# Kernel tuning notes

Measured on AMD Instinct MI355X. Metric: run time of the kernel, lower is better.

## Reference

```python
import jax, jax.numpy as jnp
import numpy as np

# decoded layout constants
NN, NO, SD = 16, 8, 4          # num_neighbors, num_obstacles, state_dim_per_agent
B = 131072                      # batch rows
H1, E, HP, AD = 64, 16, 64, 2   # phi hidden, embed, psi hidden, action dim
D_ROBOT, D_OBST = 0.3, 0.3
B_GAMMA, B_EXPH = 0.05, 1.0
PHI_MIN, PHI_MAX = -2.0, 2.0
A_MAX = 2.0


def setup_inputs() -> dict:
    key = jax.random.key(0)
    kx, kw = jax.random.split(key)
    # x: [count | goal(SD) | NN neighbor rel-states (SD each) | NO obstacle rel-pos (2 each)]
    x = jax.random.normal(kx, (B, 1 + SD + SD * NN + 2 * NO), dtype=jnp.float32) * 2.0
    x = x.at[:, 0].set(float(NN))
    names = [("Wp1n", (SD, H1)), ("bp1n", (H1,)), ("Wp2n", (H1, E)), ("bp2n", (E,)),
             ("Wr1n", (E, H1)), ("br1n", (H1,)), ("Wr2n", (H1, E)), ("br2n", (E,)),
             ("Wp1o", (2, H1)), ("bp1o", (H1,)), ("Wp2o", (H1, E)), ("bp2o", (E,)),
             ("Wr1o", (E, H1)), ("br1o", (H1,)), ("Wr2o", (H1, E)), ("br2o", (E,)),
             ("Wpsi1", (2 * E + SD, HP)), ("bpsi1", (HP,)), ("Wpsi2", (HP, AD)), ("bpsi2", (AD,))]
    ks = jax.random.split(kw, len(names))
    inp = {"x": x}
    for (n, sh), k in zip(names, ks):
        s = 1.0 / np.sqrt(sh[0])  # torch Linear default init scale
        inp[n] = jax.random.uniform(k, sh, jnp.float32, -s, s)
    return inp


def _mlp2(h, W1, b1, W2, b2):
    # Feedforward: activation between layers, linear output
    return jax.nn.relu(h @ W1 + b1) @ W2 + b2


def _deepset(el, Wp1, bp1, Wp2, bp2, Wr1, br1, Wr2, br2):
    # el: [B, n, d] -> phi each element, sum over set, rho
    phi = _mlp2(el, Wp1, bp1, Wp2, bp2)          # [B, n, E]
    return _mlp2(phi.sum(axis=1), Wr1, br1, Wr2, br2)  # [B, E]


def _barrier_sum(P, D):
    # P: [B, n, 2]; APF barrier gamma * P / (|P| * (|P|-D)^exph), summed over n
    nrm = jnp.linalg.norm(P, axis=-1, keepdims=True)   # [B, n, 1]
    H = nrm - D
    return (B_GAMMA * P / (nrm * H ** B_EXPH)).sum(axis=1)  # [B, 2]


def reference(x, Wp1n, bp1n, Wp2n, bp2n, Wr1n, br1n, Wr2n, br2n,
              Wp1o, bp1o, Wp2o, bp2o, Wr1o, br1o, Wr2o, br2o,
              Wpsi1, bpsi1, Wpsi2, bpsi2):
    nb = x.shape[0]
    g = x[:, 1:1 + SD]                                        # goal
    nbr = x[:, 1 + SD:1 + SD + SD * NN].reshape(nb, NN, SD)   # neighbor rel-states
    obs = x[:, 1 + SD + SD * NN:].reshape(nb, NO, 2)          # obstacle rel-pos

    rho_n = _deepset(nbr, Wp1n, bp1n, Wp2n, bp2n, Wr1n, br1n, Wr2n, br2n)
    rho_o = _deepset(obs, Wp1o, bp1o, Wp2o, bp2o, Wr1o, br1o, Wr2o, br2o)

    h = jnp.concatenate([rho_n, rho_o, g], axis=1)            # [B, 2E+SD]
    emp = _mlp2(h, Wpsi1, bpsi1, Wpsi2, bpsi2)                # psi network
    emp = (jnp.tanh(emp) + 1.0) / 2.0 * (PHI_MAX - PHI_MIN) + PHI_MIN  # scale_empty

    bar = _barrier_sum(-nbr[:, :, :2], D_ROBOT) + _barrier_sum(-obs, D_OBST)

    action = emp + bar
    # scale(): divide rows whose inf-norm exceeds a_max
    inv_alpha = jnp.maximum(jnp.max(jnp.abs(action), axis=1, keepdims=True) / A_MAX, 1.0)
    return action / inv_alpha
```

## Files before the change

### kernel.cpp

```cpp
#include <hip/hip_runtime.h>
#include <math.h>


typedef __attribute__((ext_vector_type(8))) _Float16 f16x8;
typedef __attribute__((ext_vector_type(2))) __fp16 fp16x2;
typedef __attribute__((ext_vector_type(4))) float f32x4;

#define XW 85

#define FR_S1N  0
#define FR_S1O  4
#define FR_G2N  8
#define FR_G2O  10
#define FR_RNA  12
#define FR_RNB  16
#define FR_ROA  18
#define FR_ROB  22
#define FR_PSI1 24
#define FR_PSI2 32
#define N_FRAGS 34

#define BIG_STR 144
#define PHI_STR 80
#define CAT_STR 144
#define L_BIG 0
#define L_PHI 2304
#define L_CAT 3584
#define L_OUT 5888
#define L_BAR 6016
#define WAVE_LDS 6144

__device__ __forceinline__ float fast_rcp(float x)  { return __builtin_amdgcn_rcpf(x); }
__device__ __forceinline__ float fast_sqrt(float x) { return __builtin_amdgcn_sqrtf(x); }

__device__ __forceinline__ float two_tanh(float a) {
    float ax = fabsf(a);
    float e = __expf(2.0f * ax);
    float t = 1.0f - 2.0f * fast_rcp(e + 1.0f);
    return copysignf(2.0f * t, a);
}

__device__ __forceinline__ void lds_fence() {
    __asm__ __volatile__("s_waitcnt lgkmcnt(0)" ::: "memory");
}

__device__ __forceinline__ unsigned pk2(float a, float b) {
    union { fp16x2 h; unsigned u; } t;
    t.h = __builtin_amdgcn_cvt_pkrtz(a, b);
    return t.u;
}
__device__ __forceinline__ f16x8 make_a4(float f0, float f1, float f2, float f3) {
    union { unsigned u[4]; f16x8 v; } U;
    U.u[0] = pk2(f0, f1); U.u[1] = pk2(f2, f3); U.u[2] = 0; U.u[3] = 0;
    return U.v;
}
__device__ __forceinline__ f16x8 make_a2(float f0, float f1) {
    union { unsigned u[4]; f16x8 v; } U;
    U.u[0] = pk2(f0, f1); U.u[1] = 0; U.u[2] = 0; U.u[3] = 0;
    return U.v;
}
__device__ __forceinline__ f16x8 lds_af(const char* area, int stride, int off, int lane) {
    int mm = lane & 15, qq = lane >> 4;
    return *(const f16x8*)(area + mm * stride + off + qq * 16);
}
__device__ __forceinline__ f16x8 load_bh(const _Float16* wsf, int frag, int lane) {
    return ((const f16x8*)(wsf + (size_t)frag * 512))[lane];
}
__device__ __forceinline__ f32x4 cinit(float b) {
    f32x4 c; c[0] = b; c[1] = b; c[2] = b; c[3] = b; return c;
}
__device__ __forceinline__ f32x4 mfma1(f16x8 a, f16x8 b, f32x4 c) {
    return __builtin_amdgcn_mfma_f32_16x16x32_f16(a, b, c, 0, 0, 0);
}

__global__ void bn_prep(const float* __restrict__ Wp1n, const float* __restrict__ Wp2n,
                        const float* __restrict__ Wr1n, const float* __restrict__ Wr2n,
                        const float* __restrict__ Wp1o, const float* __restrict__ Wp2o,
                        const float* __restrict__ Wr1o, const float* __restrict__ Wr2o,
                        const float* __restrict__ Wpsi1, const float* __restrict__ Wpsi2,
                        _Float16* __restrict__ wsf)
{
    int f = blockIdx.x;
    int lane = threadIdx.x;
    const float* W; int K, N, kk = 0, nt = 0, rel;
    if (f < 4)        { W = Wp1n;  K = 4;  N = 64; nt = f; }
    else if (f < 8)   { W = Wp1o;  K = 2;  N = 64; nt = f - 4; }
    else if (f < 10)  { W = Wp2n;  K = 64; N = 16; kk = f - 8; }
    else if (f < 12)  { W = Wp2o;  K = 64; N = 16; kk = f - 10; }
    else if (f < 16)  { W = Wr1n;  K = 16; N = 64; nt = f - 12; }
    else if (f < 18)  { W = Wr2n;  K = 64; N = 16; kk = f - 16; }
    else if (f < 22)  { W = Wr1o;  K = 16; N = 64; nt = f - 18; }
    else if (f < 24)  { W = Wr2o;  K = 64; N = 16; kk = f - 22; }
    else if (f < 32)  { rel = f - 24; W = Wpsi1; K = 36; N = 64; kk = rel >> 2; nt = rel & 3; }
    else              { W = Wpsi2; K = 64; N = 2;  kk = f - 32; }

    int q = lane >> 4, c = lane & 15;
    _Float16* dst = wsf + (size_t)f * 512 + lane * 8;
    for (int j = 0; j < 8; ++j) {
        int k = kk * 32 + q * 8 + j;
        int n = nt * 16 + c;
        float v = (k < K && n < N) ? W[k * N + n] : 0.f;
        dst[j] = (_Float16)v;
    }
}

__global__ __launch_bounds__(256) void bn_main(
    const float* __restrict__ x, const _Float16* __restrict__ wsf,
    const float* __restrict__ bp1n, const float* __restrict__ bp2n,
    const float* __restrict__ br1n, const float* __restrict__ br2n,
    const float* __restrict__ bp1o, const float* __restrict__ bp2o,
    const float* __restrict__ br1o, const float* __restrict__ br2o,
    const float* __restrict__ bpsi1, const float* __restrict__ bpsi2,
    float* __restrict__ out, int nb)
{
    __shared__ char smem[4 * WAVE_LDS];
    const int lane = threadIdx.x & 63;
    const int wid  = threadIdx.x >> 6;
    const int group = blockIdx.x * 4 + wid;
    const int row0 = group * 16;
    if (row0 >= nb) return;

    char* Wl   = smem + wid * WAVE_LDS;
    char* BIG  = Wl + L_BIG;
    char* PHI  = Wl + L_PHI;
    char* CAT  = Wl + L_CAT;
    char* OUTA = Wl + L_OUT;
    char* BAR  = Wl + L_BAR;

    const int m = lane & 15, q = lane >> 4, c = m;
    const bool q1b = (q & 1), q2b = (q & 2);

    for (int i = lane; i < 128; i += 64) {
        int r = i >> 3, d = i & 7;
        *(unsigned*)(PHI + r * PHI_STR + 32 + d * 4) = 0;
    }
    for (int i = lane; i < 256; i += 64) {
        int r = i >> 4, d = i & 15;
        *(unsigned*)(CAT + r * CAT_STR + 64 + d * 4) = 0;
    }
    lds_fence();

    {
        const float* xb = x + (size_t)(row0 + m) * XW;
        float bx = 0.f, by = 0.f;
        #pragma unroll
        for (int i = 0; i < 4; ++i) {
            int n = 4 * q + i;
            float px = -xb[5 + 4 * n], py = -xb[6 + 4 * n];
            float nrm = fast_sqrt(px * px + py * py);
            float coef = 0.05f * fast_rcp(nrm * (nrm - 0.3f));
            bx = fmaf(coef, px, bx);
            by = fmaf(coef, py, by);
        }
        #pragma unroll
        for (int i = 0; i < 2; ++i) {
            int o = 2 * q + i;
            float px = -xb[69 + 2 * o], py = -xb[70 + 2 * o];
            float nrm = fast_sqrt(px * px + py * py);
            float coef = 0.05f * fast_rcp(nrm * (nrm - 0.3f));
            bx = fmaf(coef, px, bx);
            by = fmaf(coef, py, by);
        }
        bx += __shfl_xor(bx, 16); by += __shfl_xor(by, 16);
        bx += __shfl_xor(bx, 32); by += __shfl_xor(by, 32);
        if (q == 0) { float2 bb; bb.x = bx; bb.y = by; *(float2*)(BAR + m * 8) = bb; }
    }

    if (lane < 16) {
        const float* xr = x + (size_t)(row0 + lane) * XW;
        uint2 gv;
        gv.x = pk2(xr[1], xr[2]);
        gv.y = pk2(xr[3], xr[4]);
        *(uint2*)(CAT + lane * CAT_STR + 64) = gv;
    }

    float b_s1n[4], b_s1o[4], b_rna[4], b_roa[4], b_p1[4];
    #pragma unroll
    for (int nt = 0; nt < 4; ++nt) {
        b_s1n[nt] = bp1n[nt * 16 + c];
        b_s1o[nt] = bp1o[nt * 16 + c];
        b_rna[nt] = br1n[nt * 16 + c];
        b_roa[nt] = br1o[nt * 16 + c];
        b_p1[nt]  = bpsi1[nt * 16 + c];
    }
    float b_g2n = 16.f * bp2n[c];
    float b_g2o = 8.f * bp2o[c];
    float b_rnb = br2n[c];
    float b_rob = br2o[c];
    float b_p2  = (c < 2) ? bpsi2[c] : 0.f;

    f16x8 Bs1n[4], Bg2n[2];
    #pragma unroll
    for (int nt = 0; nt < 4; ++nt) Bs1n[nt] = load_bh(wsf, FR_S1N + nt, lane);
    Bg2n[0] = load_bh(wsf, FR_G2N + 0, lane);
    Bg2n[1] = load_bh(wsf, FR_G2N + 1, lane);

    {
        const float* xr0 = x + (size_t)row0 * XW + 5 + 4 * m;
        float c0 = xr0[0], c1 = xr0[1], c2 = xr0[2], c3 = xr0[3];
        #pragma unroll 4
        for (int r = 0; r < 16; ++r) {
            int rn = (r + 1) & 15;
            const float* xrn = x + (size_t)(row0 + rn) * XW + 5 + 4 * m;
            float n0 = xrn[0], n1 = xrn[1], n2 = xrn[2], n3 = xrn[3];
            f16x8 A = make_a4(c0, c1, c2, c3);
            float sv[4];
            #pragma unroll
            for (int nt = 0; nt < 4; ++nt) {
                f32x4 cc = mfma1(A, Bs1n[nt], cinit(b_s1n[nt]));
                float s = fmaxf(cc[0], 0.f) + fmaxf(cc[1], 0.f)
                        + fmaxf(cc[2], 0.f) + fmaxf(cc[3], 0.f);
                s += __shfl_xor(s, 16);
                s += __shfl_xor(s, 32);
                sv[nt] = s;
            }
            float w = q2b ? (q1b ? sv[3] : sv[2]) : (q1b ? sv[1] : sv[0]);
            *(_Float16*)(BIG + r * BIG_STR + (q * 16 + c) * 2) = (_Float16)w;
            c0 = n0; c1 = n1; c2 = n2; c3 = n3;
        }
    }
    f16x8 Brna[4];
    #pragma unroll
    for (int nt = 0; nt < 4; ++nt) Brna[nt] = load_bh(wsf, FR_RNA + nt, lane);
    lds_fence();

    {
        f16x8 A0 = lds_af(BIG, BIG_STR, 0, lane);
        f16x8 A1 = lds_af(BIG, BIG_STR, 64, lane);
        f32x4 ca = mfma1(A0, Bg2n[0], cinit(b_g2n));
        f32x4 cb = mfma1(A1, Bg2n[1], cinit(0.f));
        #pragma unroll
        for (int reg = 0; reg < 4; ++reg)
            *(_Float16*)(PHI + (q * 4 + reg) * PHI_STR + c * 2) = (_Float16)(ca[reg] + cb[reg]);
    }
    f16x8 Brnb[2], Bs1o[4];
    Brnb[0] = load_bh(wsf, FR_RNB + 0, lane);
    Brnb[1] = load_bh(wsf, FR_RNB + 1, lane);
    #pragma unroll
    for (int nt = 0; nt < 4; ++nt) Bs1o[nt] = load_bh(wsf, FR_S1O + nt, lane);
    lds_fence();

    {
        f16x8 A = lds_af(PHI, PHI_STR, 0, lane);
        #pragma unroll
        for (int nt = 0; nt < 4; ++nt) {
            f32x4 cc = mfma1(A, Brna[nt], cinit(b_rna[nt]));
            #pragma unroll
            for (int reg = 0; reg < 4; ++reg)
                *(_Float16*)(BIG + (q * 4 + reg) * BIG_STR + (nt * 16 + c) * 2) = (_Float16)fmaxf(cc[reg], 0.f);
        }
    }
    f16x8 Bg2o[2];
    Bg2o[0] = load_bh(wsf, FR_G2O + 0, lane);
    Bg2o[1] = load_bh(wsf, FR_G2O + 1, lane);
    float of0[8], of1[8];
    #pragma unroll
    for (int t = 0; t < 8; ++t) {
        const float* xo = x + (size_t)(row0 + 2 * t + (m >> 3)) * XW + 69 + 2 * (m & 7);
        of0[t] = xo[0]; of1[t] = xo[1];
    }
    lds_fence();

    {
        f16x8 A0 = lds_af(BIG, BIG_STR, 0, lane);
        f16x8 A1 = lds_af(BIG, BIG_STR, 64, lane);
        f32x4 ca = mfma1(A0, Brnb[0], cinit(b_rnb));
        f32x4 cb = mfma1(A1, Brnb[1], cinit(0.f));
        #pragma unroll
        for (int reg = 0; reg < 4; ++reg)
            *(_Float16*)(CAT + (q * 4 + reg) * CAT_STR + c * 2) = (_Float16)(ca[reg] + cb[reg]);
    }
    f16x8 Broa[4];
    #pragma unroll
    for (int nt = 0; nt < 4; ++nt) Broa[nt] = load_bh(wsf, FR_ROA + nt, lane);
    lds_fence();

    {
        #pragma unroll
        for (int t = 0; t < 8; ++t) {
            f16x8 A = make_a2(of0[t], of1[t]);
            float sv[4];
            #pragma unroll
            for (int nt = 0; nt < 4; ++nt) {
                f32x4 cc = mfma1(A, Bs1o[nt], cinit(b_s1o[nt]));
                float s = fmaxf(cc[0], 0.f) + fmaxf(cc[1], 0.f)
                        + fmaxf(cc[2], 0.f) + fmaxf(cc[3], 0.f);
                s += __shfl_xor(s, 16);
                sv[nt] = s;
            }
            float w1 = q1b ? sv[1] : sv[0];
            float w2 = q1b ? sv[3] : sv[2];
            char* p = BIG + (2 * t + (q >> 1)) * BIG_STR + ((q & 1) * 16 + c) * 2;
            *(_Float16*)(p)      = (_Float16)w1;
            *(_Float16*)(p + 64) = (_Float16)w2;
        }
    }
    f16x8 Brob[2];
    Brob[0] = load_bh(wsf, FR_ROB + 0, lane);
    Brob[1] = load_bh(wsf, FR_ROB + 1, lane);
    lds_fence();

    {
        f16x8 A0 = lds_af(BIG, BIG_STR, 0, lane);
        f16x8 A1 = lds_af(BIG, BIG_STR, 64, lane);
        f32x4 ca = mfma1(A0, Bg2o[0], cinit(b_g2o));
        f32x4 cb = mfma1(A1, Bg2o[1], cinit(0.f));
        #pragma unroll
        for (int reg = 0; reg < 4; ++reg)
            *(_Float16*)(PHI + (q * 4 + reg) * PHI_STR + c * 2) = (_Float16)(ca[reg] + cb[reg]);
    }
    f16x8 Bp1a[4];
    #pragma unroll
    for (int nt = 0; nt < 4; ++nt) Bp1a[nt] = load_bh(wsf, FR_PSI1 + nt, lane);
    lds_fence();

    {
        f16x8 A = lds_af(PHI, PHI_STR, 0, lane);
        #pragma unroll
        for (int nt = 0; nt < 4; ++nt) {
            f32x4 cc = mfma1(A, Broa[nt], cinit(b_roa[nt]));
            #pragma unroll
            for (int reg = 0; reg < 4; ++reg)
                *(_Float16*)(BIG + (q * 4 + reg) * BIG_STR + (nt * 16 + c) * 2) = (_Float16)fmaxf(cc[reg], 0.f);
        }
    }
    f16x8 Bp1b[4], Bp2[2];
    #pragma unroll
    for (int nt = 0; nt < 4; ++nt) Bp1b[nt] = load_bh(wsf, FR_PSI1 + 4 + nt, lane);
    Bp2[0] = load_bh(wsf, FR_PSI2 + 0, lane);
    Bp2[1] = load_bh(wsf, FR_PSI2 + 1, lane);
    lds_fence();

    {
        f16x8 A0 = lds_af(BIG, BIG_STR, 0, lane);
        f16x8 A1 = lds_af(BIG, BIG_STR, 64, lane);
        f32x4 ca = mfma1(A0, Brob[0], cinit(b_rob));
        f32x4 cb = mfma1(A1, Brob[1], cinit(0.f));
        #pragma unroll
        for (int reg = 0; reg < 4; ++reg)
            *(_Float16*)(CAT + (q * 4 + reg) * CAT_STR + (16 + c) * 2) = (_Float16)(ca[reg] + cb[reg]);
    }
    lds_fence();

    {
        f16x8 A0 = lds_af(CAT, CAT_STR, 0, lane);
        f16x8 A1 = lds_af(CAT, CAT_STR, 64, lane);
        #pragma unroll
        for (int nt = 0; nt < 4; ++nt) {
            f32x4 ca = mfma1(A0, Bp1a[nt], cinit(b_p1[nt]));
            f32x4 cb = mfma1(A1, Bp1b[nt], cinit(0.f));
            #pragma unroll
            for (int reg = 0; reg < 4; ++reg)
                *(_Float16*)(BIG + (q * 4 + reg) * BIG_STR + (nt * 16 + c) * 2) = (_Float16)fmaxf(ca[reg] + cb[reg], 0.f);
        }
    }
    lds_fence();

    {
        f16x8 A0 = lds_af(BIG, BIG_STR, 0, lane);
        f16x8 A1 = lds_af(BIG, BIG_STR, 64, lane);
        f32x4 ca = mfma1(A0, Bp2[0], cinit(b_p2));
        f32x4 cb = mfma1(A1, Bp2[1], cinit(0.f));
        if (c < 2) {
            #pragma unroll
            for (int reg = 0; reg < 4; ++reg)
                *(float*)(OUTA + (q * 4 + reg) * 8 + c * 4) = ca[reg] + cb[reg];
        }
    }
    lds_fence();

    if (lane < 16) {
        float2 a  = *(const float2*)(OUTA + lane * 8);
        float2 bb = *(const float2*)(BAR + lane * 8);
        float a0 = two_tanh(a.x) + bb.x;
        float a1 = two_tanh(a.y) + bb.y;
        float amax = fmaxf(fabsf(a0), fabsf(a1));
        float inv_alpha = fmaxf(amax * 0.5f, 1.0f);
        float rr = fast_rcp(inv_alpha);
        float2 o; o.x = a0 * rr; o.y = a1 * rr;
        *(float2*)(out + (size_t)(row0 + lane) * 2) = o;
    }
}

extern "C" void kernel_launch(void* const* d_in, const int* in_sizes, int n_in,
                              void* d_out, int out_size, void* d_ws, size_t ws_size,
                              hipStream_t stream) {
    const float* x     = (const float*)d_in[0];
    const float* Wp1n  = (const float*)d_in[1];
    const float* bp1n  = (const float*)d_in[2];
    const float* Wp2n  = (const float*)d_in[3];
    const float* bp2n  = (const float*)d_in[4];
    const float* Wr1n  = (const float*)d_in[5];
    const float* br1n  = (const float*)d_in[6];
    const float* Wr2n  = (const float*)d_in[7];
    const float* br2n  = (const float*)d_in[8];
    const float* Wp1o  = (const float*)d_in[9];
    const float* bp1o  = (const float*)d_in[10];
    const float* Wp2o  = (const float*)d_in[11];
    const float* bp2o  = (const float*)d_in[12];
    const float* Wr1o  = (const float*)d_in[13];
    const float* br1o  = (const float*)d_in[14];
    const float* Wr2o  = (const float*)d_in[15];
    const float* br2o  = (const float*)d_in[16];
    const float* Wpsi1 = (const float*)d_in[17];
    const float* bpsi1 = (const float*)d_in[18];
    const float* Wpsi2 = (const float*)d_in[19];
    const float* bpsi2 = (const float*)d_in[20];
    float* out = (float*)d_out;

    int nb = in_sizes[0] / XW;
    _Float16* wsf = (_Float16*)d_ws;

    bn_prep<<<N_FRAGS, 64, 0, stream>>>(Wp1n, Wp2n, Wr1n, Wr2n,
                                        Wp1o, Wp2o, Wr1o, Wr2o,
                                        Wpsi1, Wpsi2, wsf);

    int groups = (nb + 15) / 16;
    int blocks = (groups + 3) / 4;
    bn_main<<<blocks, 256, 0, stream>>>(x, wsf,
                                        bp1n, bp2n, br1n, br2n,
                                        bp1o, bp2o, br1o, br2o,
                                        bpsi1, bpsi2, out, nb);
}
```

Baseline: 158.6 us.

## Deepen neighbor-row prefetch, drop explicit LDS waits, use 8-wave blocks

```diff
diff --git a/kernel.cpp b/kernel.cpp
--- a/kernel.cpp
+++ b/kernel.cpp
@@ -7,6 +7,7 @@
 typedef __attribute__((ext_vector_type(4))) float f32x4;
 
 #define XW 85
+#define WPB 8
 
 #define FR_S1N  0
 #define FR_S1O  4
@@ -40,8 +41,8 @@
     return copysignf(2.0f * t, a);
 }
 
-__device__ __forceinline__ void lds_fence() {
-    __asm__ __volatile__("s_waitcnt lgkmcnt(0)" ::: "memory");
+__device__ __forceinline__ void lds_order() {
+    __asm__ __volatile__("" ::: "memory");
 }
 
 __device__ __forceinline__ unsigned pk2(float a, float b) {
@@ -104,7 +105,7 @@
     }
 }
 
-__global__ __launch_bounds__(256) void bn_main(
+__global__ __launch_bounds__(512) void bn_main(
     const float* __restrict__ x, const _Float16* __restrict__ wsf,
     const float* __restrict__ bp1n, const float* __restrict__ bp2n,
     const float* __restrict__ br1n, const float* __restrict__ br2n,
@@ -113,10 +114,10 @@
     const float* __restrict__ bpsi1, const float* __restrict__ bpsi2,
     float* __restrict__ out, int nb)
 {
-    __shared__ char smem[4 * WAVE_LDS];
+    __shared__ char smem[WPB * WAVE_LDS];
     const int lane = threadIdx.x & 63;
     const int wid  = threadIdx.x >> 6;
-    const int group = blockIdx.x * 4 + wid;
+    const int group = blockIdx.x * WPB + wid;
     const int row0 = group * 16;
     if (row0 >= nb) return;
 
@@ -138,7 +139,7 @@
         int r = i >> 4, d = i & 15;
         *(unsigned*)(CAT + r * CAT_STR + 64 + d * 4) = 0;
     }
-    lds_fence();
+    lds_order();
 
     {
         const float* xb = x + (size_t)(row0 + m) * XW;
@@ -196,14 +197,21 @@
     Bg2n[1] = load_bh(wsf, FR_G2N + 1, lane);
 
     {
-        const float* xr0 = x + (size_t)row0 * XW + 5 + 4 * m;
-        float c0 = xr0[0], c1 = xr0[1], c2 = xr0[2], c3 = xr0[3];
+        float buf[4][4];
+        #pragma unroll
+        for (int i = 0; i < 4; ++i) {
+            const float* xi = x + (size_t)(row0 + i) * XW + 5 + 4 * m;
+            buf[i][0] = xi[0]; buf[i][1] = xi[1]; buf[i][2] = xi[2]; buf[i][3] = xi[3];
+        }
         #pragma unroll 4
         for (int r = 0; r < 16; ++r) {
-            int rn = (r + 1) & 15;
-            const float* xrn = x + (size_t)(row0 + rn) * XW + 5 + 4 * m;
-            float n0 = xrn[0], n1 = xrn[1], n2 = xrn[2], n3 = xrn[3];
-            f16x8 A = make_a4(c0, c1, c2, c3);
+            int sl = r & 3;
+            f16x8 A = make_a4(buf[sl][0], buf[sl][1], buf[sl][2], buf[sl][3]);
+            if (r + 4 < 16) {
+                const float* xn = x + (size_t)(row0 + r + 4) * XW + 5 + 4 * m;
+                buf[sl][0] = xn[0]; buf[sl][1] = xn[1];
+                buf[sl][2] = xn[2]; buf[sl][3] = xn[3];
+            }
             float sv[4];
             #pragma unroll
             for (int nt = 0; nt < 4; ++nt) {
@@ -216,13 +224,12 @@
             }
             float w = q2b ? (q1b ? sv[3] : sv[2]) : (q1b ? sv[1] : sv[0]);
             *(_Float16*)(BIG + r * BIG_STR + (q * 16 + c) * 2) = (_Float16)w;
-            c0 = n0; c1 = n1; c2 = n2; c3 = n3;
         }
     }
     f16x8 Brna[4];
     #pragma unroll
     for (int nt = 0; nt < 4; ++nt) Brna[nt] = load_bh(wsf, FR_RNA + nt, lane);
-    lds_fence();
+    lds_order();
 
     {
         f16x8 A0 = lds_af(BIG, BIG_STR, 0, lane);
@@ -238,7 +245,7 @@
     Brnb[1] = load_bh(wsf, FR_RNB + 1, lane);
     #pragma unroll
     for (int nt = 0; nt < 4; ++nt) Bs1o[nt] = load_bh(wsf, FR_S1O + nt, lane);
-    lds_fence();
+    lds_order();
 
     {
         f16x8 A = lds_af(PHI, PHI_STR, 0, lane);
@@ -259,7 +266,7 @@
         const float* xo = x + (size_t)(row0 + 2 * t + (m >> 3)) * XW + 69 + 2 * (m & 7);
         of0[t] = xo[0]; of1[t] = xo[1];
     }
-    lds_fence();
+    lds_order();
 
     {
         f16x8 A0 = lds_af(BIG, BIG_STR, 0, lane);
@@ -273,7 +280,7 @@
     f16x8 Broa[4];
     #pragma unroll
     for (int nt = 0; nt < 4; ++nt) Broa[nt] = load_bh(wsf, FR_ROA + nt, lane);
-    lds_fence();
+    lds_order();
 
     {
         #pragma unroll
@@ -298,7 +305,7 @@
     f16x8 Brob[2];
     Brob[0] = load_bh(wsf, FR_ROB + 0, lane);
     Brob[1] = load_bh(wsf, FR_ROB + 1, lane);
-    lds_fence();
+    lds_order();
 
     {
         f16x8 A0 = lds_af(BIG, BIG_STR, 0, lane);
@@ -312,7 +319,7 @@
     f16x8 Bp1a[4];
     #pragma unroll
     for (int nt = 0; nt < 4; ++nt) Bp1a[nt] = load_bh(wsf, FR_PSI1 + nt, lane);
-    lds_fence();
+    lds_order();
 
     {
         f16x8 A = lds_af(PHI, PHI_STR, 0, lane);
@@ -329,7 +336,7 @@
     for (int nt = 0; nt < 4; ++nt) Bp1b[nt] = load_bh(wsf, FR_PSI1 + 4 + nt, lane);
     Bp2[0] = load_bh(wsf, FR_PSI2 + 0, lane);
     Bp2[1] = load_bh(wsf, FR_PSI2 + 1, lane);
-    lds_fence();
+    lds_order();
 
     {
         f16x8 A0 = lds_af(BIG, BIG_STR, 0, lane);
@@ -340,7 +347,7 @@
         for (int reg = 0; reg < 4; ++reg)
             *(_Float16*)(CAT + (q * 4 + reg) * CAT_STR + (16 + c) * 2) = (_Float16)(ca[reg] + cb[reg]);
     }
-    lds_fence();
+    lds_order();
 
     {
         f16x8 A0 = lds_af(CAT, CAT_STR, 0, lane);
@@ -354,7 +361,7 @@
                 *(_Float16*)(BIG + (q * 4 + reg) * BIG_STR + (nt * 16 + c) * 2) = (_Float16)fmaxf(ca[reg] + cb[reg], 0.f);
         }
     }
-    lds_fence();
+    lds_order();
 
     {
         f16x8 A0 = lds_af(BIG, BIG_STR, 0, lane);
@@ -367,7 +374,7 @@
                 *(float*)(OUTA + (q * 4 + reg) * 8 + c * 4) = ca[reg] + cb[reg];
         }
     }
-    lds_fence();
+    lds_order();
 
     if (lane < 16) {
         float2 a  = *(const float2*)(OUTA + lane * 8);
@@ -416,8 +423,8 @@
                                         Wpsi1, Wpsi2, wsf);
 
     int groups = (nb + 15) / 16;
-    int blocks = (groups + 3) / 4;
-    bn_main<<<blocks, 256, 0, stream>>>(x, wsf,
+    int blocks = (groups + WPB - 1) / WPB;
+    bn_main<<<blocks, 512, 0, stream>>>(x, wsf,
                                         bp1n, bp2n, br1n, br2n,
                                         bp1o, bp2o, br1o, br2o,
                                         bpsi1, bpsi2, out, nb);
```

Result: slower. 165.5 us (+4.3%).
